# Optimization experiments

Measured on AMD Instinct MI355X. Metric: run time of the kernel, lower is better.

## Reference

```python
import jax, jax.numpy as jnp
import numpy as np

B, L_PROG = 8, 12
NUM_CLASSES, NUM_ATTRS = 256, 256
MAX_CONCEPTS, MAX_OBJECTS = 4096, 128
N_ATTR_PER_OBJ = 8
E, A, H = 64, 64, 256  # embed_dim, attention_dim, hidden_dim


def setup_inputs() -> dict:
    key = jax.random.key(0)
    ks = jax.random.split(key, 22)
    f = lambda k, shape: jax.random.normal(k, shape, dtype=jnp.float32) * 0.05
    return {
        'class_embIn': f(ks[0], (NUM_CLASSES, E)),
        'class_embOut': f(ks[1], (NUM_CLASSES, E)),
        'attr_embIn': f(ks[2], (NUM_ATTRS, E)),
        'attr_embOut': f(ks[3], (NUM_ATTRS, E)),
        'concept_embIn': f(ks[4], (MAX_CONCEPTS, E)),
        'concept_embOut': f(ks[5], (MAX_CONCEPTS, E)),
        'meta_init': f(ks[6], (A,)),
        'object_init': f(ks[7], (E,)),
        'attention_init': f(ks[8], (A,)),
        'axon_w1': f(ks[9], (A + E, H)), 'axon_b1': f(ks[10], (H,)),
        'axon_w2': f(ks[11], (H, E)), 'axon_b2': f(ks[12], (E,)),
        'meta_w1': f(ks[13], (E + A, H)), 'meta_b1': f(ks[14], (H,)),
        'meta_w2': f(ks[15], (H, A)), 'meta_b2': f(ks[16], (A,)),
        'program_ops': jax.random.randint(ks[17], (B, L_PROG), 0, 3),
        'program_args': jax.random.randint(ks[18], (B, L_PROG), 0, MAX_CONCEPTS),
        'gt_classes': jax.random.randint(ks[19], (B, MAX_OBJECTS), 0, NUM_CLASSES),
        'gt_attributes': jax.random.randint(ks[20], (B, MAX_OBJECTS, N_ATTR_PER_OBJ), 0, NUM_ATTRS),
    }


def _mlp(x, w1, b1, w2, b2):
    return jnp.maximum(x @ w1 + b1, 0.0) @ w2 + b2


def reference(class_embIn, class_embOut, attr_embIn, attr_embOut,
              concept_embIn, concept_embOut, meta_init, object_init,
              attention_init, axon_w1, axon_b1, axon_w2, axon_b2,
              meta_w1, meta_b1, meta_w2, meta_b2,
              program_ops, program_args, gt_classes, gt_attributes):
    Bb, Lp = program_ops.shape
    C = concept_embIn.shape[0]
    N = C + gt_classes.shape[1]  # dim_concept = max_concepts + max_objects

    # object embeddings: class embedding + sum of attribute embeddings  (B, O, E)
    objIn = class_embIn[gt_classes] + attr_embIn[gt_attributes].sum(axis=2)
    objOut = class_embOut[gt_classes] + attr_embOut[gt_attributes].sum(axis=2)

    # thought = [concepts ; objects]  (B, N, E)
    thoughtIn = jnp.concatenate(
        [jnp.broadcast_to(concept_embIn[None], (Bb, C, E)), objIn], axis=1)
    thoughtOut = jnp.concatenate(
        [jnp.broadcast_to(concept_embOut[None], (Bb, C, E)), objOut], axis=1)

    args_emb = concept_embOut[program_args]          # (B, L, E)
    is_mode = (program_ops == 0).astype(jnp.float32)     # (B, L)
    is_insert = (program_ops == 1).astype(jnp.float32)
    is_transfer = (program_ops == 2).astype(jnp.float32)

    meta0 = jnp.broadcast_to(meta_init[None], (Bb, A))
    att0 = jnp.broadcast_to(attention_init[None, None], (Bb, N, A))

    def step(carry, xs):
        meta, attention = carry
        m, ins, tr, arg = xs  # (B,), (B,), (B,), (B,E)
        new_meta = _mlp(jnp.concatenate([meta, arg], axis=-1),
                        meta_w1, meta_b1, meta_w2, meta_b2)
        meta = m[:, None] * new_meta + (1.0 - m[:, None]) * meta
        # insert: meta scaled by mean_e(arg * thoughtOut)
        proj = (arg[:, None, :] * thoughtOut).mean(axis=-1)        # (B, N)
        att_insert = meta[:, None, :] * proj[:, :, None]           # (B, N, A)
        # transfer: bilinear scores thoughtIn . axon, mean-aggregate attention
        mb = jnp.broadcast_to(meta[:, None, :], (Bb, N, A))
        axon = _mlp(jnp.concatenate([thoughtOut, mb], axis=-1),
                    axon_w1, axon_b1, axon_w2, axon_b2)            # (B, N, E)
        scores = jnp.einsum('bje,bke->bjk', thoughtIn, axon)       # (B, N, N)
        att_transfer = jnp.einsum('bjk,bka->bja', scores, attention) / N
        attention = attention + ins[:, None, None] * att_insert \
                              + tr[:, None, None] * att_transfer
        return (meta, attention), None

    xs = (is_mode.T, is_insert.T, is_transfer.T,
          jnp.transpose(args_emb, (1, 0, 2)))
    (meta, attention), _ = jax.lax.scan(step, (meta0, att0), xs)

    output_length = jnp.mean(attention ** 2, axis=-1)              # (B, N)
    return jax.nn.log_softmax(output_length, axis=1)
```

## Files before the change

kernel.cpp:

```cpp
#include <hip/hip_runtime.h>
#include <hip/hip_bf16.h>

typedef __hip_bfloat16 bf16;
typedef float f32x4 __attribute__((ext_vector_type(4)));
typedef short s16x8 __attribute__((ext_vector_type(8)));

#define B_    8
#define LP    12
#define NC    4096
#define NO    128
#define NAPO  8
#define NN    4224
#define E_    64
#define A_    64
#define H_    256
#define QC    80
#define PROJ0 65
#define NCHUNK 17

#define TOT_IN 688896
#define QTF_C  67584
#define QTF_B  337920
#define TB_P   983040

struct Ptr16 { const void* p[16]; };
union U8 { s16x8 v; unsigned u[4]; };

__device__ __forceinline__ float b2f(bf16 x){ return __bfloat162float(x); }
__device__ __forceinline__ float bs2f(unsigned short s){
  union { unsigned u; float f; } x; x.u = ((unsigned)s) << 16; return x.f;
}
__device__ __forceinline__ unsigned short f2bs(float f){
  bf16 h = __float2bfloat16(f);
  union { bf16 h; unsigned short s; } x; x.h = h; return x.s;
}
__device__ __forceinline__ unsigned pack2(float a, float b){
  return (unsigned)f2bs(a) | ((unsigned)f2bs(b) << 16);
}
__device__ __forceinline__ float lo16f(unsigned w){
  union { unsigned u; float f; } x; x.u = w << 16; return x.f;
}
__device__ __forceinline__ float hi16f(unsigned w){
  union { unsigned u; float f; } x; x.u = w & 0xffff0000u; return x.f;
}
__device__ __forceinline__ float rdval(const void* p, int i, int fl){
  return fl ? ((const float*)p)[i] : bs2f(((const unsigned short*)p)[i]);
}

__global__ void k_prep(Ptr16 ps, int* flag, float* dst,
                       unsigned short* awFrag,
                       const int* gtc, const int* gta,
                       float* objIn, float* objOut, float* qsum_esum){
  int tid = threadIdx.x;
  const unsigned short* u = (const unsigned short*)ps.p[4];
  int hit = (((u[tid*16] >> 7) & 0xFF) >= 137) ? 1 : 0;
  unsigned long long m = __ballot(hit);
  int fl = (m != 0ULL) ? 1 : 0;
  int mb = blockIdx.x;
  if (mb < 2691){
    int idx = mb*256 + tid;
    if (idx >= TOT_IN) return;
    constexpr int cum[17] = {0,16384,32768,49152,65536,327680,589824,589888,589952,
                             622720,622976,639360,639424,672192,672448,688832,688896};
    int t = 0;
    #pragma unroll
    for (int i=1;i<16;i++) if (idx >= cum[i]) t = i;
    dst[idx] = rdval(ps.p[t], idx - cum[t], fl);
  } else if (mb < 2755){
    int idx = (mb-2691)*256 + tid;
    int j = idx & 7;
    int lane = (idx >> 3) & 63;
    int mm = (idx >> 9) & 15;
    int kc = idx >> 13;
    int e = kc*32 + (lane>>4)*8 + j;
    int h = mm*16 + (lane&15);
    awFrag[idx] = f2bs(rdval(ps.p[8], e*H_ + h, fl));
  } else if (mb < 3011){
    int idx = (mb-2755)*256 + tid;
    int e = idx & 63; int bo = idx >> 6;
    int cls = gtc[bo];
    float vi = rdval(ps.p[0], cls*E_ + e, fl);
    float vo = rdval(ps.p[1], cls*E_ + e, fl);
    const int* ga = gta + bo*NAPO;
    #pragma unroll
    for (int j=0;j<NAPO;j++){
      int at = ga[j];
      vi += rdval(ps.p[2], at*E_ + e, fl);
      vo += rdval(ps.p[3], at*E_ + e, fl);
    }
    objIn[idx] = vi; objOut[idx] = vo;
  } else {
    if (tid < 656) qsum_esum[tid] = 0.f;
    if (tid == 0) *flag = fl;
  }
}

__device__ __forceinline__ void mid_meta(char* smem, int b,
                       const float* conceptOut, const float* meta_init,
                       const float* mw1, const float* mb1, const float* mw2, const float* mb2,
                       const float* aw1, const float* ab1,
                       const int* ops, const int* args,
                       float* metaAll, float* metaH){
  unsigned* mw1p = (unsigned*)smem;
  unsigned* mw2p = (unsigned*)(smem + 65536);
  unsigned* aw1p = (unsigned*)(smem + 98304);
  float* meta_s  = (float*)(smem + 131072);
  float* argx    = (float*)(smem + 131328);
  float* hid     = (float*)(smem + 131584);
  float* part    = (float*)(smem + 132608);
  int tid = threadIdx.x;

  for (int i=tid; i<64*256; i+=256){
    int j2 = i >> 8, t = i & 255;
    mw1p[i] = pack2(mw1[(2*j2)*H_ + t], mw1[(2*j2+1)*H_ + t]);
  }
  for (int i=tid; i<128*64; i+=256){
    int h2 = i >> 6, a = i & 63;
    mw2p[i] = pack2(mw2[(2*h2)*A_ + a], mw2[(2*h2+1)*A_ + a]);
  }
  for (int i=tid; i<32*256; i+=256){
    int a2 = i >> 8, t = i & 255;
    aw1p[i] = pack2(aw1[(E_+2*a2)*H_ + t], aw1[(E_+2*a2+1)*H_ + t]);
  }
  float r_mb1 = mb1[tid];
  float r_ab1 = ab1[tid];
  float r_mb2 = (tid < A_) ? mb2[tid] : 0.f;
  if (tid < A_) meta_s[tid] = meta_init[tid];
  __syncthreads();

  for (int t=0;t<LP;t++){
    int op  = ops[b*LP + t];
    int arg = args[b*LP + t];
    if (tid >= 64 && tid < 128) argx[tid-64] = conceptOut[arg*E_ + (tid-64)];
    __syncthreads();
    float acc = r_mb1;
    for (int j2=0;j2<32;j2++){
      unsigned w = mw1p[j2*256 + tid];
      float2 xp = *(const float2*)&meta_s[2*j2];
      acc = fmaf(xp.x, lo16f(w), acc);
      acc = fmaf(xp.y, hi16f(w), acc);
    }
    for (int j2=0;j2<32;j2++){
      unsigned w = mw1p[(32+j2)*256 + tid];
      float2 xp = *(const float2*)&argx[2*j2];
      acc = fmaf(xp.x, lo16f(w), acc);
      acc = fmaf(xp.y, hi16f(w), acc);
    }
    hid[tid] = fmaxf(acc, 0.f);
    __syncthreads();
    int wv_ = tid >> 6, l = tid & 63;
    float acc2 = 0.f;
    for (int h2 = wv_*32; h2 < wv_*32+32; h2++){
      unsigned w = mw2p[h2*64 + l];
      float2 hp = *(const float2*)&hid[2*h2];
      acc2 = fmaf(hp.x, lo16f(w), acc2);
      acc2 = fmaf(hp.y, hi16f(w), acc2);
    }
    part[wv_*64 + l] = acc2;
    __syncthreads();
    if (tid < A_){
      float s = part[tid] + part[64+tid] + part[128+tid] + part[192+tid] + r_mb2;
      float nm = (op==0) ? s : meta_s[tid];
      meta_s[tid] = nm;
      metaAll[(b*LP+t)*A_ + tid] = nm;
    }
    __syncthreads();
    float mh = r_ab1;
    for (int a2=0;a2<32;a2++){
      unsigned w = aw1p[a2*256 + tid];
      float2 mp = *(const float2*)&meta_s[2*a2];
      mh = fmaf(mp.x, lo16f(w), mh);
      mh = fmaf(mp.y, hi16f(w), mh);
    }
    metaH[(b*LP+t)*H_ + tid] = mh;
  }
}

__device__ __forceinline__ void mid_qt(char* smem, int idx,
                       const float* conceptIn, const float* conceptOut, const int* args,
                       const float* objIn, const float* objOut,
                       unsigned short* QTf, float* qsum){
  float* tile = (float*)smem;
  float* argv = (float*)(smem + 66560);
  float* qs   = (float*)(smem + 69632);
  int b = idx / NCHUNK, chunk = idx % NCHUNK;
  int tid = threadIdx.x;
  int rows = (chunk < 16) ? 256 : 128;
  int n0 = chunk*256;
  int n = n0 + tid;
  bool valid = (tid < rows);
  if (tid < 80) qs[tid] = 0.f;
  unsigned short* Qb = QTf + (size_t)b*QTF_B + ((n>>5)*512 + (n&31));
  {
    const float* src = (chunk < 16) ? (conceptIn + (size_t)n0*E_) : (objIn + (size_t)b*NO*E_);
    int tot = rows*64;
    for (int i=tid; i<tot; i+=256) tile[(i>>6)*65 + (i&63)] = src[i];
  }
  __syncthreads();
  if (valid){
    Qb[0] = 0x3F80;
    Qb[4*QTF_C + 13*32] = 0;
    Qb[4*QTF_C + 14*32] = 0;
    Qb[4*QTF_C + 15*32] = 0;
    for (int e=0;e<64;e++){
      int qc = 1+e;
      Qb[(qc>>4)*QTF_C + (qc&15)*32] = f2bs(tile[tid*65 + e]);
    }
    for (int i=0;i<64;i++){
      int e = (i + tid) & 63;
      atomicAdd(&qs[1+e], tile[tid*65+e]);
    }
  }
  __syncthreads();
  for (int i=tid;i<LP*E_;i+=256) argv[i] = conceptOut[args[b*LP + (i>>6)]*E_ + (i&63)];
  {
    const float* src = (chunk < 16) ? (conceptOut + (size_t)n0*E_) : (objOut + (size_t)b*NO*E_);
    int tot = rows*64;
    for (int i=tid; i<tot; i+=256) tile[(i>>6)*65 + (i&63)] = src[i];
  }
  __syncthreads();
  float dots[LP];
  #pragma unroll
  for (int t=0;t<LP;t++) dots[t] = 0.f;
  for (int e=0;e<64;e++){
    float o = tile[tid*65 + e];
    #pragma unroll
    for (int t=0;t<LP;t++) dots[t] += o*argv[t*64+e];
  }
  #pragma unroll
  for (int t=0;t<LP;t++){
    float v = valid ? dots[t]*(1.f/E_) : 0.f;
    if (valid){
      int qc = PROJ0+t;
      Qb[(qc>>4)*QTF_C + (qc&15)*32] = f2bs(v);
    }
    float r = v;
    #pragma unroll
    for (int off=32; off>0; off>>=1) r += __shfl_down(r, off, 64);
    if ((tid & 63) == 0) atomicAdd(&qs[PROJ0+t], r);
  }
  __syncthreads();
  if (tid < 80) atomicAdd(&qsum[b*QC + tid], qs[tid]);
  if (chunk == 0 && tid == 0) atomicAdd(&qsum[b*QC], (float)NN);
}

__device__ __forceinline__ void mid_base(int blk,
                       const float* conceptOut, const float* objOut,
                       const unsigned short* awFrag,
                       unsigned short* AoptC, unsigned short* AoptO){
  int n0 = blk * 64;
  int tid = threadIdx.x;
  int w = tid >> 6, l = tid & 63, quad = l >> 4, lq = l & 15;
  int n = n0 + w*16 + lq;
  const float* src = (n < NC) ? (conceptOut + (size_t)n*E_) : (objOut + (size_t)(n-NC)*E_);
  f32x4 acc[16];
  #pragma unroll
  for (int m=0;m<16;m++) acc[m] = (f32x4){0.f,0.f,0.f,0.f};
  #pragma unroll
  for (int kc=0;kc<2;kc++){
    s16x8 bfr;
    #pragma unroll
    for (int j=0;j<8;j++) bfr[j] = (short)f2bs(src[kc*32 + quad*8 + j]);
    const unsigned short* ap = awFrag + ((size_t)(kc*16)*64 + l)*8;
    #pragma unroll
    for (int m=0;m<16;m++){
      s16x8 af = *(const s16x8*)(ap + (size_t)m*64*8);
      acc[m] = __builtin_amdgcn_mfma_f32_16x16x32_bf16(af, bfr, acc[m], 0, 0, 0);
    }
  }
  int nl = n & 31;
  if (n < NC){
    int nch = n >> 5;
    #pragma unroll
    for (int m=0;m<16;m++){
      #pragma unroll
      for (int r=0;r<4;r++)
        AoptC[(size_t)(m*128 + nch)*512 + (quad*4+r)*32 + nl] = f2bs(acc[m][r]);
    }
  } else {
    int no = n - NC; int bb = no >> 7; int oc = (no & 127) >> 5;
    #pragma unroll
    for (int m=0;m<16;m++){
      #pragma unroll
      for (int r=0;r<4;r++)
        AoptO[(size_t)((bb*16 + m)*4 + oc)*512 + (quad*4+r)*32 + nl] = f2bs(acc[m][r]);
    }
  }
}

__global__ __launch_bounds__(256) void k_mid(
    const float* conceptIn, const float* conceptOut,
    const float* meta_init, const float* mw1, const float* mb1, const float* mw2, const float* mb2,
    const float* aw1, const float* ab1, const int* ops, const int* args,
    const float* objIn, const float* objOut, const unsigned short* awFrag,
    float* metaAll, float* metaH, unsigned short* QTf, float* qsum,
    unsigned short* AoptC, unsigned short* AoptO){
  __shared__ __align__(16) char smem[133888];
  int mb = blockIdx.x;
  if (mb < 8)
    mid_meta(smem, mb, conceptOut, meta_init, mw1, mb1, mw2, mb2, aw1, ab1, ops, args, metaAll, metaH);
  else if (mb < 144)
    mid_qt(smem, mb-8, conceptIn, conceptOut, args, objIn, objOut, QTf, qsum);
  else
    mid_base(mb-144, conceptOut, objOut, awFrag, AoptC, AoptO);
}

__global__ __launch_bounds__(64) void k_T(const unsigned short* AoptC, const unsigned short* AoptO,
                                          const unsigned short* QTf, const float* metaH,
                                          unsigned* TB){
  int bid = blockIdx.x;
  int kh = bid & 7; int ht = (bid >> 3) & 3; int bt = bid >> 5; int b = bt / LP;
  int l = threadIdx.x, quad = l >> 4, lq = l & 15;
  int off = lq*32 + quad*8;
  int start = (kh < 4) ? (kh*17) : (68 + (kh-4)*16);
  int count = (kh < 4) ? 17 : 16;
  float mh[4];
  #pragma unroll
  for (int s=0;s<4;s++) mh[s] = metaH[(size_t)bt*H_ + ht*64 + s*16 + lq];
  f32x4 acc[4][5];
  #pragma unroll
  for (int s=0;s<4;s++){
    #pragma unroll
    for (int c=0;c<5;c++) acc[s][c] = (f32x4){0.f,0.f,0.f,0.f};
  }
  const unsigned short* QTb = QTf + (size_t)b*QTF_B + off;
  const unsigned short* AC  = AoptC + (size_t)(ht*4)*65536 + off;
  const unsigned short* AO  = AoptO + (size_t)(b*16 + ht*4)*2048 + off;
  for (int it=0; it<count; it++){
    int nchunk = start + it;
    U8 bfr[5];
    #pragma unroll
    for (int c=0;c<5;c++)
      bfr[c].v = *(const s16x8*)(QTb + (size_t)c*QTF_C + (size_t)nchunk*512);
    bool isC = (nchunk < 128);
    #pragma unroll
    for (int s=0;s<4;s++){
      U8 a;
      a.v = isC ? *(const s16x8*)(AC + (size_t)s*65536 + (size_t)nchunk*512)
                : *(const s16x8*)(AO + (size_t)s*2048 + (size_t)(nchunk-128)*512);
      float mhs = mh[s];
      U8 af;
      #pragma unroll
      for (int d=0;d<4;d++){
        unsigned wv = a.u[d];
        float lo = fmaxf(__uint_as_float(wv << 16) + mhs, 0.f);
        float hi = fmaxf(__uint_as_float(wv & 0xffff0000u) + mhs, 0.f);
        af.u[d] = __builtin_amdgcn_perm(__float_as_uint(hi), __float_as_uint(lo), 0x07060302u);
      }
      #pragma unroll
      for (int c=0;c<5;c++)
        acc[s][c] = __builtin_amdgcn_mfma_f32_16x16x32_bf16(af.v, bfr[c].v, acc[s][c], 0, 0, 0);
    }
  }
  unsigned* Tp = TB + (size_t)kh*TB_P + ((size_t)bt*4 + ht)*2560;
  #pragma unroll
  for (int s=0;s<4;s++){
    #pragma unroll
    for (int c=0;c<5;c++){
      uint2 v;
      v.x = pack2(acc[s][c][0], acc[s][c][1]);
      v.y = pack2(acc[s][c][2], acc[s][c][3]);
      *(uint2*)(Tp + (s*5+c)*128 + l*2) = v;
    }
  }
}

__global__ __launch_bounds__(256) void k_U(const unsigned* TB,
                                           const float* w2, const float* b2v,
                                           const float* qsum, float* Ut0, float* Ut1){
  __shared__ float Wt[128*64];
  __shared__ float Tt[128*81];
  int bid = blockIdx.x;
  int kq = bid & 1; int bt = bid >> 1; int b = bt / LP;
  int tid = threadIdx.x;
  for (int i=tid; i<8192; i+=256){
    int hl = i >> 6, e = i & 63;
    Wt[i] = w2[(kq*128 + hl)*E_ + e];
  }
  #pragma unroll
  for (int half=0; half<2; half++){
    const unsigned* base = TB + ((size_t)bt*4 + kq*2 + half)*2560;
    for (int i2=tid; i2<2560; i2+=256){
      float lo = 0.f, hi = 0.f;
      #pragma unroll
      for (int p=0;p<8;p++){
        unsigned w = base[(size_t)p*TB_P + i2];
        lo += lo16f(w); hi += hi16f(w);
      }
      int idx = 2*i2;
      int sc = idx >> 8; int ll = (idx >> 2) & 63; int r = idx & 3;
      int s = sc/5, c = sc - s*5;
      int hl = half*64 + s*16 + ((ll>>4)<<2) + r;
      int qc = c*16 + (ll&15);
      Tt[hl*81 + qc]     = lo;
      Tt[(hl+1)*81 + qc] = hi;
    }
  }
  __syncthreads();
  int el = tid & 15, ql = tid >> 4;
  float acc[4][5];
  #pragma unroll
  for (int i=0;i<4;i++){
    #pragma unroll
    for (int j=0;j<5;j++) acc[i][j]=0.f;
  }
  #pragma unroll 4
  for (int kk=0; kk<128; kk++){
    float4 wv = *(const float4*)&Wt[kk*64 + el*4];
    float ww[4] = {wv.x, wv.y, wv.z, wv.w};
    const float* tp = &Tt[kk*81 + ql*5];
    #pragma unroll
    for (int j=0;j<5;j++){
      float tv = tp[j];
      #pragma unroll
      for (int i=0;i<4;i++) acc[i][j] = fmaf(ww[i], tv, acc[i][j]);
    }
  }
  const float invN = 1.f/NN;
  float* Up = (kq ? Ut1 : Ut0) + (size_t)bt*5120;
  if (kq == 0){
    float be[4], qv[5];
    #pragma unroll
    for (int i=0;i<4;i++) be[i] = b2v[el*4+i];
    #pragma unroll
    for (int j=0;j<5;j++) qv[j] = qsum[b*QC + ql*5+j];
    #pragma unroll
    for (int i=0;i<4;i++){
      #pragma unroll
      for (int j=0;j<5;j++)
        Up[(el*4+i)*QC + ql*5+j] = (acc[i][j] + be[i]*qv[j]) * invN;
    }
  } else {
    #pragma unroll
    for (int i=0;i<4;i++){
      #pragma unroll
      for (int j=0;j<5;j++)
        Up[(el*4+i)*QC + ql*5+j] = acc[i][j] * invN;
    }
  }
}

__global__ __launch_bounds__(256) void k_rec(const float* Ut0, const float* Ut1, const float* metaAll,
                                             const int* ops, const float* att_init, float* Cm){
  __shared__ float C[QC*65];
  __shared__ float Ul[2][64*81];
  int b = blockIdx.x, tid = threadIdx.x;
  int w = tid >> 6, l = tid & 63, quad = l >> 4, lq = l & 15;
  for (int i=tid;i<QC*65;i+=256) C[i] = 0.f;
  if (tid < A_) C[tid] = att_init[tid];
  {
    const float* U0 = Ut0 + (size_t)(b*LP)*5120;
    const float* U1 = Ut1 + (size_t)(b*LP)*5120;
    #pragma unroll
    for (int k=0;k<5;k++){
      int i = tid*4 + k*1024;
      float4 v0 = *(const float4*)&U0[i];
      float4 v1 = *(const float4*)&U1[i];
      int r = i/80, c = i%80;
      Ul[0][r*81+c]   = v0.x+v1.x; Ul[0][r*81+c+1] = v0.y+v1.y;
      Ul[0][r*81+c+2] = v0.z+v1.z; Ul[0][r*81+c+3] = v0.w+v1.w;
    }
  }
  __syncthreads();
  for (int t=0;t<LP;t++){
    float4 rv0[5], rv1[5];
    if (t < LP-1){
      const float* U0 = Ut0 + (size_t)(b*LP+t+1)*5120;
      const float* U1 = Ut1 + (size_t)(b*LP+t+1)*5120;
      #pragma unroll
      for (int k=0;k<5;k++){
        rv0[k] = *(const float4*)&U0[tid*4 + k*1024];
        rv1[k] = *(const float4*)&U1[tid*4 + k*1024];
      }
    }
    const float* Uc = Ul[t&1];
    U8 af[3][4];
    #pragma unroll
    for (int k0t=0;k0t<3;k0t++){
      #pragma unroll
      for (int s=0;s<4;s++){
        int e = s*16 + lq;
        int qb = k0t*32 + quad*8;
        float v[8];
        #pragma unroll
        for (int j=0;j<8;j++){
          int qc = qb + j;
          v[j] = (qc < QC) ? Uc[e*81 + qc] : 0.f;
        }
        #pragma unroll
        for (int d=0;d<4;d++) af[k0t][s].u[d] = pack2(v[2*d], v[2*d+1]);
      }
    }
    U8 bf[3];
    #pragma unroll
    for (int k0t=0;k0t<3;k0t++){
      int kb = k0t*32 + quad*8;
      float v[8];
      #pragma unroll
      for (int j=0;j<8;j++){
        int k = kb + j;
        v[j] = (k < QC) ? C[k*65 + w*16 + lq] : 0.f;
      }
      #pragma unroll
      for (int d=0;d<4;d++) bf[k0t].u[d] = pack2(v[2*d], v[2*d+1]);
    }
    f32x4 acc[4];
    #pragma unroll
    for (int s=0;s<4;s++){
      acc[s] = (f32x4){0.f,0.f,0.f,0.f};
      #pragma unroll
      for (int k0t=0;k0t<3;k0t++)
        acc[s] = __builtin_amdgcn_mfma_f32_16x16x32_bf16(af[k0t][s].v, bf[k0t].v, acc[s], 0, 0, 0);
    }
    int op = ops[b*LP + t];
    float tr  = (op==2) ? 1.f : 0.f;
    float ins = (op==1) ? 1.f : 0.f;
    __syncthreads();
    #pragma unroll
    for (int s=0;s<4;s++){
      #pragma unroll
      for (int r=0;r<4;r++){
        int e = s*16 + quad*4 + r;
        C[(1+e)*65 + w*16 + lq] += tr*acc[s][r];
      }
    }
    if (tid < A_) C[(PROJ0+t)*65 + tid] += ins*metaAll[(b*LP+t)*A_ + tid];
    if (t < LP-1){
      float* Un = Ul[(t+1)&1];
      #pragma unroll
      for (int k=0;k<5;k++){
        int i = tid*4 + k*1024;
        int r = i/80, c = i%80;
        Un[r*81+c]   = rv0[k].x+rv1[k].x; Un[r*81+c+1] = rv0[k].y+rv1[k].y;
        Un[r*81+c+2] = rv0[k].z+rv1[k].z; Un[r*81+c+3] = rv0[k].w+rv1[k].w;
      }
    }
    __syncthreads();
  }
  for (int i=tid;i<QC*A_;i+=256) Cm[b*QC*A_ + i] = C[(i>>6)*65 + (i&63)];
}

__global__ __launch_bounds__(128) void k_out(const unsigned short* QTf, const float* Cm,
                                             float* ol, float* esum){
  __shared__ float C[QC*A_];
  __shared__ float wsum[2];
  int b = blockIdx.x / 33, rem = blockIdx.x % 33;
  int tid = threadIdx.x;
  for (int i=tid;i<QC*A_;i+=128) C[i] = Cm[b*QC*A_ + i];
  __syncthreads();
  int n = rem*128 + tid;
  float y[A_];
  #pragma unroll
  for (int a=0;a<A_;a++) y[a]=0.f;
  const unsigned short* Qb = QTf + (size_t)b*QTF_B + ((n>>5)*512 + (n&31));
  for (int j=0;j<QC;j++){
    float qvv = bs2f(Qb[(j>>4)*QTF_C + (j&15)*32]);
    const float* Cj = &C[j*A_];
    #pragma unroll
    for (int a=0;a<A_;a++) y[a] = fmaf(qvv, Cj[a], y[a]);
  }
  float s = 0.f;
  #pragma unroll
  for (int a=0;a<A_;a++) s = fmaf(y[a], y[a], s);
  float o = s * (1.f/A_);
  ol[(size_t)b*NN + n] = o;
  float contrib = expf(o);
  #pragma unroll
  for (int off=32; off>0; off>>=1) contrib += __shfl_down(contrib, off, 64);
  if ((tid & 63) == 0) wsum[tid>>6] = contrib;
  __syncthreads();
  if (tid == 0) atomicAdd(&esum[b], wsum[0]+wsum[1]);
}

__global__ void k_fin(const float* ol, const float* esum, const int* flag, void* out){
  int idx = blockIdx.x*256 + threadIdx.x;
  if (idx < B_*NN){
    int b = idx / NN;
    float v = ol[idx] - logf(esum[b]);
    if (*flag) ((float*)out)[idx] = v;
    else       ((bf16*)out)[idx]  = __float2bfloat16(v);
  }
}

extern "C" void kernel_launch(void* const* d_in, const int* in_sizes, int n_in,
                              void* d_out, int out_size, void* d_ws, size_t ws_size,
                              hipStream_t stream) {
  (void)in_sizes; (void)n_in; (void)out_size; (void)ws_size;
  const int* ops  = (const int*)d_in[17];
  const int* args = (const int*)d_in[18];
  const int* gtc  = (const int*)d_in[19];
  const int* gta  = (const int*)d_in[20];

  float* ws = (float*)d_ws;
  int* flag = (int*)ws;
  float* W  = ws + 16;

  const float* conceptIn  = W + 65536;
  const float* conceptOut = W + 327680;
  const float* meta_init  = W + 589824;
  const float* att_init   = W + 589888;
  const float* aw1        = W + 589952;
  const float* ab1        = W + 622720;
  const float* aw2        = W + 622976;
  const float* ab2        = W + 639360;
  const float* mw1        = W + 639424;
  const float* mb1        = W + 672192;
  const float* mw2        = W + 672448;
  const float* mb2        = W + 688832;

  constexpr size_t OFF_OBJIN   = 16 + TOT_IN;
  constexpr size_t OFF_OBJOUT  = OFF_OBJIN  + 65536;
  constexpr size_t OFF_METAALL = OFF_OBJOUT + 65536;
  constexpr size_t OFF_METAH   = OFF_METAALL + 6144;
  constexpr size_t OFF_QSUM    = OFF_METAH  + 24576;
  constexpr size_t OFF_ESUM    = OFF_QSUM   + 640;
  constexpr size_t OFF_UT0     = OFF_ESUM   + 16;
  constexpr size_t OFF_UT1     = OFF_UT0    + 491520;
  constexpr size_t OFF_CM      = OFF_UT1    + 491520;
  constexpr size_t OFF_OL      = OFF_CM     + 40960;
  constexpr size_t OFF_QTF     = OFF_OL     + 33792;
  constexpr size_t OFF_AOPTC   = OFF_QTF    + 1351680;
  constexpr size_t OFF_AOPTO   = OFF_AOPTC  + 524288;
  constexpr size_t OFF_AWF     = OFF_AOPTO  + 131072;
  constexpr size_t OFF_TB      = OFF_AWF    + 8192;

  float* objIn   = ws + OFF_OBJIN;
  float* objOut  = ws + OFF_OBJOUT;
  float* metaAll = ws + OFF_METAALL;
  float* metaH   = ws + OFF_METAH;
  float* qsum    = ws + OFF_QSUM;
  float* esum    = ws + OFF_ESUM;
  float* Ut0     = ws + OFF_UT0;
  float* Ut1     = ws + OFF_UT1;
  float* Cm      = ws + OFF_CM;
  float* ol      = ws + OFF_OL;
  unsigned short* QTf    = (unsigned short*)(ws + OFF_QTF);
  unsigned short* AoptC  = (unsigned short*)(ws + OFF_AOPTC);
  unsigned short* AoptO  = (unsigned short*)(ws + OFF_AOPTO);
  unsigned short* awFrag = (unsigned short*)(ws + OFF_AWF);
  unsigned* TB           = (unsigned*)(ws + OFF_TB);

  Ptr16 ps;
  const int src_idx[16] = {0,1,2,3,4,5,6,8,9,10,11,12,13,14,15,16};
  for (int i=0;i<16;i++) ps.p[i] = d_in[src_idx[i]];

  k_prep<<<3012, 256, 0, stream>>>(ps, flag, W, awFrag, gtc, gta, objIn, objOut, qsum);
  k_mid <<<224, 256, 0, stream>>>(conceptIn, conceptOut, meta_init, mw1, mb1, mw2, mb2,
                                  aw1, ab1, ops, args, objIn, objOut, awFrag,
                                  metaAll, metaH, QTf, qsum, AoptC, AoptO);
  k_T   <<<B_*LP*4*8, 64, 0, stream>>>(AoptC, AoptO, QTf, metaH, TB);
  k_U   <<<B_*LP*2, 256, 0, stream>>>(TB, aw2, ab2, qsum, Ut0, Ut1);
  k_rec <<<B_, 256, 0, stream>>>(Ut0, Ut1, metaAll, ops, att_init, Cm);
  k_out <<<B_*33, 128, 0, stream>>>(QTf, Cm, ol, esum);
  k_fin <<<(B_*NN + 255)/256, 256, 0, stream>>>(ol, esum, flag, d_out);
}
```

Baseline: 265.4 us.

## Precompute qsum column sums in prep and fuse final log-softmax into k_out

Column sums of the concept and object embeddings are now reduced in k_prep (new blocks for concept rows, shared-memory partials for objects), and the projection sums are derived algebraically from those sums and the argument embeddings in a small new k_mid branch. This replaces the per-element shared atomics in mid_qt. The final normalization kernel is removed: the last k_out block per batch, detected with an atomic counter, writes the normalized output. In exchange it adds a hipMemsetAsync launch and a serial tail done by one block per batch.

```diff
diff --git a/kernel.cpp b/kernel.cpp
--- a/kernel.cpp
+++ b/kernel.cpp
@@ -47,16 +47,18 @@
   return fl ? ((const float*)p)[i] : bs2f(((const unsigned short*)p)[i]);
 }
 
+
 __global__ void k_prep(Ptr16 ps, int* flag, float* dst,
                        unsigned short* awFrag,
                        const int* gtc, const int* gta,
-                       float* objIn, float* objOut, float* qsum_esum){
+                       float* objIn, float* objOut, float* qsum){
   int tid = threadIdx.x;
   const unsigned short* u = (const unsigned short*)ps.p[4];
   int hit = (((u[tid*16] >> 7) & 0xFF) >= 137) ? 1 : 0;
   unsigned long long m = __ballot(hit);
   int fl = (m != 0ULL) ? 1 : 0;
   int mb = blockIdx.x;
+  float* acc = qsum + 640;
   if (mb < 2691){
     int idx = mb*256 + tid;
     if (idx >= TOT_IN) return;
@@ -76,6 +78,9 @@
     int h = mm*16 + (lane&15);
     awFrag[idx] = f2bs(rdval(ps.p[8], e*H_ + h, fl));
   } else if (mb < 3011){
+    __shared__ float ls[128];
+    if (tid < 128) ls[tid] = 0.f;
+    __syncthreads();
     int idx = (mb-2755)*256 + tid;
     int e = idx & 63; int bo = idx >> 6;
     int cls = gtc[bo];
@@ -89,9 +94,34 @@
       vo += rdval(ps.p[3], at*E_ + e, fl);
     }
     objIn[idx] = vi; objOut[idx] = vo;
+    atomicAdd(&ls[e], vi);
+    atomicAdd(&ls[64+e], vo);
+    __syncthreads();
+    int b = (mb - 2755) >> 5;
+    float* objsumIn  = acc + 144;
+    float* objsumOut = acc + 656;
+    if (tid < 64) atomicAdd(&objsumIn[b*64+tid], ls[tid]);
+    else if (tid < 128) atomicAdd(&objsumOut[b*64+(tid-64)], ls[tid]);
   } else {
-    if (tid < 656) qsum_esum[tid] = 0.f;
-    if (tid == 0) *flag = fl;
+    int j = mb - 3011;
+    __shared__ float ls[128];
+    if (tid < 128) ls[tid] = 0.f;
+    __syncthreads();
+    int e = tid & 63, r0 = tid >> 6;
+    float si = 0.f, so = 0.f;
+    for (int rr = r0; rr < 128; rr += 4){
+      int row = j*128 + rr;
+      si += rdval(ps.p[4], row*E_ + e, fl);
+      so += rdval(ps.p[5], row*E_ + e, fl);
+    }
+    atomicAdd(&ls[e], si);
+    atomicAdd(&ls[64+e], so);
+    __syncthreads();
+    float* csumIn  = acc + 16;
+    float* csumOut = acc + 80;
+    if (tid < 64) atomicAdd(&csumIn[tid], ls[tid]);
+    else if (tid < 128) atomicAdd(&csumOut[tid-64], ls[tid]);
+    if (j == 0 && tid == 0) *flag = fl;
   }
 }
 
@@ -179,17 +209,15 @@
 __device__ __forceinline__ void mid_qt(char* smem, int idx,
                        const float* conceptIn, const float* conceptOut, const int* args,
                        const float* objIn, const float* objOut,
-                       unsigned short* QTf, float* qsum){
+                       unsigned short* QTf){
   float* tile = (float*)smem;
   float* argv = (float*)(smem + 66560);
-  float* qs   = (float*)(smem + 69632);
   int b = idx / NCHUNK, chunk = idx % NCHUNK;
   int tid = threadIdx.x;
   int rows = (chunk < 16) ? 256 : 128;
   int n0 = chunk*256;
   int n = n0 + tid;
   bool valid = (tid < rows);
-  if (tid < 80) qs[tid] = 0.f;
   unsigned short* Qb = QTf + (size_t)b*QTF_B + ((n>>5)*512 + (n&31));
   {
     const float* src = (chunk < 16) ? (conceptIn + (size_t)n0*E_) : (objIn + (size_t)b*NO*E_);
@@ -206,10 +234,6 @@
       int qc = 1+e;
       Qb[(qc>>4)*QTF_C + (qc&15)*32] = f2bs(tile[tid*65 + e]);
     }
-    for (int i=0;i<64;i++){
-      int e = (i + tid) & 63;
-      atomicAdd(&qs[1+e], tile[tid*65+e]);
-    }
   }
   __syncthreads();
   for (int i=tid;i<LP*E_;i+=256) argv[i] = conceptOut[args[b*LP + (i>>6)]*E_ + (i&63)];
@@ -219,29 +243,21 @@
     for (int i=tid; i<tot; i+=256) tile[(i>>6)*65 + (i&63)] = src[i];
   }
   __syncthreads();
-  float dots[LP];
-  #pragma unroll
-  for (int t=0;t<LP;t++) dots[t] = 0.f;
-  for (int e=0;e<64;e++){
-    float o = tile[tid*65 + e];
-    #pragma unroll
-    for (int t=0;t<LP;t++) dots[t] += o*argv[t*64+e];
-  }
-  #pragma unroll
-  for (int t=0;t<LP;t++){
-    float v = valid ? dots[t]*(1.f/E_) : 0.f;
-    if (valid){
+  if (valid){
+    float dots[LP];
+    #pragma unroll
+    for (int t=0;t<LP;t++) dots[t] = 0.f;
+    for (int e=0;e<64;e++){
+      float o = tile[tid*65 + e];
+      #pragma unroll
+      for (int t=0;t<LP;t++) dots[t] += o*argv[t*64+e];
+    }
+    #pragma unroll
+    for (int t=0;t<LP;t++){
       int qc = PROJ0+t;
-      Qb[(qc>>4)*QTF_C + (qc&15)*32] = f2bs(v);
-    }
-    float r = v;
-    #pragma unroll
-    for (int off=32; off>0; off>>=1) r += __shfl_down(r, off, 64);
-    if ((tid & 63) == 0) atomicAdd(&qs[PROJ0+t], r);
-  }
-  __syncthreads();
-  if (tid < 80) atomicAdd(&qsum[b*QC + tid], qs[tid]);
-  if (chunk == 0 && tid == 0) atomicAdd(&qsum[b*QC], (float)NN);
+      Qb[(qc>>4)*QTF_C + (qc&15)*32] = f2bs(dots[t]*(1.f/E_));
+    }
+  }
 }
 
 __device__ __forceinline__ void mid_base(int blk,
@@ -285,6 +301,28 @@
       for (int r=0;r<4;r++)
         AoptO[(size_t)((bb*16 + m)*4 + oc)*512 + (quad*4+r)*32 + nl] = f2bs(acc[m][r]);
     }
+  }
+}
+
+__device__ __forceinline__ void mid_qsumfin(int b, const float* conceptOut, const int* args,
+                                            float* qsum){
+  int tid = threadIdx.x;
+  if (tid >= 64) return;
+  float* acc = qsum + 640;
+  const float* csumIn    = acc + 16;
+  const float* csumOut   = acc + 80;
+  const float* objsumIn  = acc + 144;
+  const float* objsumOut = acc + 656;
+  if (tid == 0) qsum[b*QC] = (float)NN;
+  qsum[b*QC + 1 + tid] = csumIn[tid] + objsumIn[b*64+tid];
+  if (tid < 3) qsum[b*QC + 77 + tid] = 0.f;
+  float cot = csumOut[tid] + objsumOut[b*64+tid];
+  for (int t=0;t<LP;t++){
+    float av = conceptOut[args[b*LP+t]*E_ + tid];
+    float r = cot * av;
+    #pragma unroll
+    for (int off=32; off>0; off>>=1) r += __shfl_down(r, off, 64);
+    if (tid == 0) qsum[b*QC + PROJ0 + t] = r * (1.f/E_);
   }
 }
 
@@ -300,9 +338,11 @@
   if (mb < 8)
     mid_meta(smem, mb, conceptOut, meta_init, mw1, mb1, mw2, mb2, aw1, ab1, ops, args, metaAll, metaH);
   else if (mb < 144)
-    mid_qt(smem, mb-8, conceptIn, conceptOut, args, objIn, objOut, QTf, qsum);
+    mid_qt(smem, mb-8, conceptIn, conceptOut, args, objIn, objOut, QTf);
+  else if (mb < 224)
+    mid_base(mb-144, conceptOut, objOut, awFrag, AoptC, AoptO);
   else
-    mid_base(mb-144, conceptOut, objOut, awFrag, AoptC, AoptO);
+    mid_qsumfin(mb-224, conceptOut, args, qsum);
 }
 
 __global__ __launch_bounds__(64) void k_T(const unsigned short* AoptC, const unsigned short* AoptO,
@@ -541,9 +581,11 @@
 }
 
 __global__ __launch_bounds__(128) void k_out(const unsigned short* QTf, const float* Cm,
-                                             float* ol, float* esum){
+                                             float* ol, float* esum, const int* flag, void* out){
   __shared__ float C[QC*A_];
   __shared__ float wsum[2];
+  __shared__ bool last;
+  unsigned* cnt = (unsigned*)(esum + 8);
   int b = blockIdx.x / 33, rem = blockIdx.x % 33;
   int tid = threadIdx.x;
   for (int i=tid;i<QC*A_;i+=128) C[i] = Cm[b*QC*A_ + i];
@@ -569,16 +611,25 @@
   for (int off=32; off>0; off>>=1) contrib += __shfl_down(contrib, off, 64);
   if ((tid & 63) == 0) wsum[tid>>6] = contrib;
   __syncthreads();
-  if (tid == 0) atomicAdd(&esum[b], wsum[0]+wsum[1]);
-}
-
-__global__ void k_fin(const float* ol, const float* esum, const int* flag, void* out){
-  int idx = blockIdx.x*256 + threadIdx.x;
-  if (idx < B_*NN){
-    int b = idx / NN;
-    float v = ol[idx] - logf(esum[b]);
-    if (*flag) ((float*)out)[idx] = v;
-    else       ((bf16*)out)[idx]  = __float2bfloat16(v);
+  if (tid == 0){
+    atomicAdd(&esum[b], wsum[0]+wsum[1]);
+    __threadfence();
+    unsigned old = atomicAdd(&cnt[b], 1u);
+    last = (old == 32u);
+  }
+  __syncthreads();
+  if (last){
+    __threadfence();
+    float es = esum[b];
+    float lsm = logf(es);
+    const float* olb = ol + (size_t)b*NN;
+    if (*flag){
+      float* op_ = (float*)out + (size_t)b*NN;
+      for (int i=tid;i<NN;i+=128) op_[i] = olb[i] - lsm;
+    } else {
+      bf16* op_ = (bf16*)out + (size_t)b*NN;
+      for (int i=tid;i<NN;i+=128) op_[i] = __float2bfloat16(olb[i] - lsm);
+    }
   }
 }
 
@@ -614,7 +665,7 @@
   constexpr size_t OFF_METAH   = OFF_METAALL + 6144;
   constexpr size_t OFF_QSUM    = OFF_METAH  + 24576;
   constexpr size_t OFF_ESUM    = OFF_QSUM   + 640;
-  constexpr size_t OFF_UT0     = OFF_ESUM   + 16;
+  constexpr size_t OFF_UT0     = OFF_ESUM   + 1168;
   constexpr size_t OFF_UT1     = OFF_UT0    + 491520;
   constexpr size_t OFF_CM      = OFF_UT1    + 491520;
   constexpr size_t OFF_OL      = OFF_CM     + 40960;
@@ -640,17 +691,18 @@
   unsigned short* awFrag = (unsigned short*)(ws + OFF_AWF);
   unsigned* TB           = (unsigned*)(ws + OFF_TB);
 
+  hipMemsetAsync(esum, 0, 1168*sizeof(float), stream);
+
   Ptr16 ps;
   const int src_idx[16] = {0,1,2,3,4,5,6,8,9,10,11,12,13,14,15,16};
   for (int i=0;i<16;i++) ps.p[i] = d_in[src_idx[i]];
 
-  k_prep<<<3012, 256, 0, stream>>>(ps, flag, W, awFrag, gtc, gta, objIn, objOut, qsum);
-  k_mid <<<224, 256, 0, stream>>>(conceptIn, conceptOut, meta_init, mw1, mb1, mw2, mb2,
+  k_prep<<<3043, 256, 0, stream>>>(ps, flag, W, awFrag, gtc, gta, objIn, objOut, qsum);
+  k_mid <<<232, 256, 0, stream>>>(conceptIn, conceptOut, meta_init, mw1, mb1, mw2, mb2,
                                   aw1, ab1, ops, args, objIn, objOut, awFrag,
                                   metaAll, metaH, QTf, qsum, AoptC, AoptO);
   k_T   <<<B_*LP*4*8, 64, 0, stream>>>(AoptC, AoptO, QTf, metaH, TB);
   k_U   <<<B_*LP*2, 256, 0, stream>>>(TB, aw2, ab2, qsum, Ut0, Ut1);
   k_rec <<<B_, 256, 0, stream>>>(Ut0, Ut1, metaAll, ops, att_init, Cm);
-  k_out <<<B_*33, 128, 0, stream>>>(QTf, Cm, ol, esum);
-  k_fin <<<(B_*NN + 255)/256, 256, 0, stream>>>(ol, esum, flag, d_out);
-}
+  k_out <<<B_*33, 128, 0, stream>>>(QTf, Cm, ol, esum, flag, d_out);
+}
```

Result: slower. 286.0 us (+7.8%).
